# Performance work log

Measured on AMD Instinct MI355X. Metric: run time of the kernel, lower is better.

Reference implementation:

```python
import jax, jax.numpy as jnp
import numpy as np

B, C_IN, N = 8, 512, 4096   # batch, input channels, timesteps
D, K = 256, 2048            # code dim (n_out), codebook size (vq_n_embed)
EMA_G = 0.99                # vq_ema_gamma


def setup_inputs() -> dict:
    key = jax.random.key(0)
    k1, k2, k3 = jax.random.split(key, 3)
    z = jax.random.normal(k1, (B, C_IN, N), jnp.float32)
    # emb: xavier_uniform with gain=10 over (K, D)
    eb = 10.0 * np.sqrt(6.0 / (K + D))
    emb = jax.random.uniform(k2, (K, D), jnp.float32, -eb, eb)
    # 1x1 Conv1d weight (no bias), xavier_uniform over (D, C_IN)
    wb = np.sqrt(6.0 / (D + C_IN))
    W = jax.random.uniform(k3, (D, C_IN), jnp.float32, -wb, wb)
    # EMA buffers as initialized in __init__
    ema_numer = emb * (1.0 - EMA_G)
    ema_denom = jnp.ones((K,), jnp.float32) * (1.0 - EMA_G)
    return {"z": z, "W": W, "emb": emb, "ema_numer": ema_numer, "ema_denom": ema_denom}


def reference(z, W, emb, ema_numer, ema_denom):
    # 1x1 conv (no bias): ze (B, D, N)
    ze = jnp.einsum('dc,bcn->bdn', W, z)
    e = jax.lax.stop_gradient(emb)  # sg(emb)
    # Squared L2 distances (B, K, N) via ||ze||^2 + ||e||^2 - 2 e.ze
    # (mathematically equal to the broadcasted (ze-e)^2 sum, without the
    #  huge (B,K,D,N) intermediate)
    ze_sq = jnp.sum(ze * ze, axis=1)              # (B, N)
    e_sq = jnp.sum(e * e, axis=1)                 # (K,)
    cross = jnp.einsum('kd,bdn->bkn', e, ze)      # (B, K, N)
    d2 = ze_sq[:, None, :] + e_sq[None, :, None] - 2.0 * cross
    min_ind = jnp.argmin(d2, axis=1)              # (B, N) int
    zq = jnp.take(e, min_ind, axis=0).transpose(0, 2, 1)  # (B, D, N)
    # ReplaceGrad straight-through: value = zq, gradient flows to ze
    out = ze + jax.lax.stop_gradient(zq - ze)
    # EMA codebook statistics (scatter-add over assignments)
    flat_ind = min_ind.reshape(-1)                          # (B*N,)
    flat_ze = ze.transpose(0, 2, 1).reshape(-1, D)          # (B*N, D)
    z_sum = jax.ops.segment_sum(flat_ze, flat_ind, num_segments=K)
    n_sum = jax.ops.segment_sum(jnp.ones((flat_ind.shape[0],), ze.dtype), flat_ind, num_segments=K)
    ema_numer_new = EMA_G * ema_numer + (1.0 - EMA_G) * z_sum
    ema_denom_new = EMA_G * ema_denom + (1.0 - EMA_G) * n_sum
    return out, ema_numer_new, ema_denom_new
```

## Files before the change

kernel.cpp:

```cpp
#include <hip/hip_runtime.h>

#define B_   8
#define CIN  512
#define NN_  4096
#define DD   256
#define KK   2048
#define KSPLIT 4
#define KPER (KK / KSPLIT)
#define NG   (B_ * NN_)

typedef _Float16 f16x8 __attribute__((ext_vector_type(8)));
typedef _Float16 f16x4 __attribute__((ext_vector_type(4)));
typedef float    f32x16 __attribute__((ext_vector_type(16)));

#define MFMA16 __builtin_amdgcn_mfma_f32_32x32x16_f16

#define GLDS16(gp, lp) __builtin_amdgcn_global_load_lds( \
    (const __attribute__((address_space(1))) void*)(gp), \
    (__attribute__((address_space(3))) void*)(lp), 16, 0, 0)

__global__ __launch_bounds__(256) void k_esq(const float* __restrict__ emb,
                                             float* __restrict__ esq,
                                             _Float16* __restrict__ emb_h,
                                             _Float16* __restrict__ emb_l) {
  int t = threadIdx.x;
  int lane = t & 63;
  int k = blockIdx.x * 4 + (t >> 6);
  float4 v = *(const float4*)&emb[(size_t)k * DD + 4 * lane];
  float s = v.x * v.x + v.y * v.y + v.z * v.z + v.w * v.w;
  f16x4 h, l;
  float* vp = (float*)&v;
#pragma unroll
  for (int i = 0; i < 4; i++) {
    _Float16 hh = (_Float16)vp[i];
    h[i] = hh;
    l[i] = (_Float16)(vp[i] - (float)hh);
  }
  *(f16x4*)&emb_h[(size_t)k * DD + 4 * lane] = h;
  *(f16x4*)&emb_l[(size_t)k * DD + 4 * lane] = l;
  for (int off = 32; off > 0; off >>= 1) s += __shfl_down(s, off, 64);
  if (lane == 0) esq[k] = s;
}

__global__ __launch_bounds__(256) void k_ze(const float* __restrict__ W,
                                            const float* __restrict__ z,
                                            _Float16* __restrict__ zeT_h,
                                            _Float16* __restrict__ zeT_l) {
  __shared__ __align__(16) char sm[67584];
  const int t = threadIdx.x;
  const int w = t >> 6, lane = t & 63;
  const int lr = lane & 31, lh = lane >> 5;
  const int wm = w & 1, wn = w >> 1;
  const int swz = (lr >> 1) & 3;
  const int b = blockIdx.z, d0 = blockIdx.y * 128, n0 = blockIdx.x * 128;
  const float* zb = z + (size_t)b * CIN * NN_ + n0;

  _Float16* Ah = (_Float16*)sm;
  _Float16* Al = (_Float16*)(sm + 16384);
  float*    Zs = (float*)(sm + 32768);

  auto stageA = [&](int buf, int c0) {
#pragma unroll
    for (int i = 0; i < 4; i++) {
      int fid = i * 256 + t;
      int d = fid >> 3, q8 = fid & 7;
      float4 v = *(const float4*)&W[(size_t)(d0 + d) * CIN + c0 + 4 * q8];
      float* vp = (float*)&v;
      f16x4 h, l;
#pragma unroll
      for (int e = 0; e < 4; e++) {
        _Float16 hh = (_Float16)vp[e];
        h[e] = hh;
        l[e] = (_Float16)(vp[e] - (float)hh);
      }
      int p16 = (q8 >> 1) ^ ((d >> 1) & 3);
      int off = (buf * 128 + d) * 32 + p16 * 8 + (q8 & 1) * 4;
      *(f16x4*)&Ah[off] = h;
      *(f16x4*)&Al[off] = l;
    }
  };
  auto stageZ = [&](int buf, int c0) {
#pragma unroll
    for (int i = 0; i < 4; i++) {
      int r = 8 * w + 2 * i;
      float* lbase = Zs + (size_t)buf * 4096 + r * 128;
      const float* gp = zb + (size_t)(c0 + r + lh) * NN_ + 4 * lr;
      GLDS16(gp, lbase);
    }
  };

  f32x16 acc[2][2];
#pragma unroll
  for (int mt = 0; mt < 2; mt++)
#pragma unroll
    for (int nt = 0; nt < 2; nt++)
#pragma unroll
      for (int i = 0; i < 16; i++) acc[mt][nt][i] = 0.0f;

  stageA(0, 0);
  stageZ(0, 0);
  int buf = 0;
  for (int c0 = 0; c0 < CIN; c0 += 32) {
    __syncthreads();
    if (c0 + 32 < CIN) { stageA(buf ^ 1, c0 + 32); stageZ(buf ^ 1, c0 + 32); }
    const _Float16* AhB = Ah + (size_t)buf * 128 * 32;
    const _Float16* AlB = Al + (size_t)buf * 128 * 32;
    const float*    ZsB = Zs + (size_t)buf * 4096;
#pragma unroll
    for (int s = 0; s < 2; s++) {
      const int cbase = 16 * s + 8 * lh;
      const int pa = (2 * s + lh) ^ swz;
      const int aoff = pa * 8;
      f16x8 ah0 = *(const f16x8*)&AhB[(wm * 64 + lr) * 32 + aoff];
      f16x8 ah1 = *(const f16x8*)&AhB[(wm * 64 + 32 + lr) * 32 + aoff];
      f16x8 al0 = *(const f16x8*)&AlB[(wm * 64 + lr) * 32 + aoff];
      f16x8 al1 = *(const f16x8*)&AlB[(wm * 64 + 32 + lr) * 32 + aoff];
      f16x8 bh0, bl0, bh1, bl1;
#pragma unroll
      for (int j = 0; j < 8; j++) {
        float x0 = ZsB[(cbase + j) * 128 + wn * 64 + lr];
        float x1 = ZsB[(cbase + j) * 128 + wn * 64 + 32 + lr];
        _Float16 h0 = (_Float16)x0;
        bh0[j] = h0;
        bl0[j] = (_Float16)(x0 - (float)h0);
        _Float16 h1 = (_Float16)x1;
        bh1[j] = h1;
        bl1[j] = (_Float16)(x1 - (float)h1);
      }
      acc[0][0] = MFMA16(ah0, bh0, acc[0][0], 0, 0, 0);
      acc[0][1] = MFMA16(ah0, bh1, acc[0][1], 0, 0, 0);
      acc[1][0] = MFMA16(ah1, bh0, acc[1][0], 0, 0, 0);
      acc[1][1] = MFMA16(ah1, bh1, acc[1][1], 0, 0, 0);
      acc[0][0] = MFMA16(ah0, bl0, acc[0][0], 0, 0, 0);
      acc[0][1] = MFMA16(ah0, bl1, acc[0][1], 0, 0, 0);
      acc[1][0] = MFMA16(ah1, bl0, acc[1][0], 0, 0, 0);
      acc[1][1] = MFMA16(ah1, bl1, acc[1][1], 0, 0, 0);
      acc[0][0] = MFMA16(al0, bh0, acc[0][0], 0, 0, 0);
      acc[0][1] = MFMA16(al0, bh1, acc[0][1], 0, 0, 0);
      acc[1][0] = MFMA16(al1, bh0, acc[1][0], 0, 0, 0);
      acc[1][1] = MFMA16(al1, bh1, acc[1][1], 0, 0, 0);
    }
    buf ^= 1;
  }

  __syncthreads();
  _Float16* Eh = (_Float16*)sm;
  _Float16* El = (_Float16*)(sm + 33792);
#pragma unroll
  for (int mt = 0; mt < 2; mt++)
#pragma unroll
    for (int nt = 0; nt < 2; nt++) {
      int n_l = wn * 64 + nt * 32 + lr;
#pragma unroll
      for (int g = 0; g < 4; g++) {
        int d_l = wm * 64 + mt * 32 + 8 * g + 4 * lh;
        f16x4 h, l;
#pragma unroll
        for (int e = 0; e < 4; e++) {
          float x = acc[mt][nt][4 * g + e];
          _Float16 hh = (_Float16)x;
          h[e] = hh;
          l[e] = (_Float16)(x - (float)hh);
        }
        *(f16x4*)&Eh[n_l * 132 + d_l] = h;
        *(f16x4*)&El[n_l * 132 + d_l] = l;
      }
    }
  __syncthreads();
  _Float16* gh = zeT_h + ((size_t)b * NN_ + n0) * DD + d0;
  _Float16* gl = zeT_l + ((size_t)b * NN_ + n0) * DD + d0;
#pragma unroll
  for (int i = 0; i < 16; i++) {
    int n = i * 8 + w * 2 + lh;
    int d = 4 * lr;
    *(f16x4*)&gh[(size_t)n * DD + d] = *(const f16x4*)&Eh[n * 132 + d];
    *(f16x4*)&gl[(size_t)n * DD + d] = *(const f16x4*)&El[n * 132 + d];
  }
}

__global__ __launch_bounds__(256) void k_argmin(const _Float16* __restrict__ emb_h,
                                                const _Float16* __restrict__ emb_l,
                                                const _Float16* __restrict__ zeT_h,
                                                const _Float16* __restrict__ zeT_l,
                                                const float* __restrict__ esq,
                                                float* __restrict__ pval,
                                                int* __restrict__ pidx) {
  __shared__ __align__(16) char sm[69632];
  const int t = threadIdx.x;
  const int w = t >> 6, lane = t & 63;
  const int lr = lane & 31, lh = lane >> 5;
  const int wm = w & 1, wn = w >> 1;
  const int swz = (lr >> 1) & 3;
  const int b = blockIdx.y, n0 = blockIdx.x * 128, ks = blockIdx.z;
  const int kbase = ks * KPER;

  float* esqs = (float*)(sm + 65536);
  *(float2*)&esqs[2 * t] = *(const float2*)&esq[kbase + 2 * t];

  const _Float16* zb_h = zeT_h + ((size_t)b * NN_ + n0) * DD;
  const _Float16* zb_l = zeT_l + ((size_t)b * NN_ + n0) * DD;

  auto stage = [&](int buf, int kt, int dc) {
    const int k0 = kbase + kt * 128;
    const int q = lane & 3, rr = lane >> 2;
    const int g = q ^ ((rr >> 1) & 3);
    const int rb0 = 32 * w;
#pragma unroll
    for (int j = 0; j < 2; j++) {
      int rb = rb0 + 16 * j;
      int r = rb + rr;
      int col = dc + 8 * g;
      size_t eo = (size_t)(k0 + r) * DD + col;
      size_t zo = (size_t)r * DD + col;
      char* lb = sm + (size_t)buf * 8192 + rb * 64;
      GLDS16(emb_h + eo, lb);
      GLDS16(emb_l + eo, lb + 16384);
      GLDS16(zb_h + zo, lb + 32768);
      GLDS16(zb_l + zo, lb + 49152);
    }
  };

  f32x16 vzero;
#pragma unroll
  for (int i = 0; i < 16; i++) vzero[i] = 0.0f;

  float bestv[2];
  int   besti[2];
  bestv[0] = bestv[1] = 3.4e38f;
  besti[0] = besti[1] = 0;

  stage(0, 0, 0);
  int buf = 0;
  for (int kt = 0; kt < 4; kt++) {
    f32x16 acc00 = vzero, acc01 = vzero, acc10 = vzero, acc11 = vzero;
    for (int dc = 0; dc < DD; dc += 32) {
      __syncthreads();
      if (dc + 32 < DD) stage(buf ^ 1, kt, dc + 32);
      else if (kt < 3) stage(buf ^ 1, kt + 1, 0);
      const _Float16* EHb = (const _Float16*)(sm + buf * 8192);
      const _Float16* ELb = (const _Float16*)(sm + 16384 + buf * 8192);
      const _Float16* ZHb = (const _Float16*)(sm + 32768 + buf * 8192);
      const _Float16* ZLb = (const _Float16*)(sm + 49152 + buf * 8192);
#pragma unroll
      for (int s = 0; s < 2; s++) {
        const int p = (2 * s + lh) ^ swz;
        const int acol = p * 8;
        const int ar0 = (wm * 64 + lr) * 32 + acol;
        const int ar1 = (wm * 64 + 32 + lr) * 32 + acol;
        const int br0 = (wn * 64 + lr) * 32 + acol;
        const int br1 = (wn * 64 + 32 + lr) * 32 + acol;
        f16x8 ah0 = *(const f16x8*)(EHb + ar0);
        f16x8 ah1 = *(const f16x8*)(EHb + ar1);
        f16x8 al0 = *(const f16x8*)(ELb + ar0);
        f16x8 al1 = *(const f16x8*)(ELb + ar1);
        f16x8 bh0 = *(const f16x8*)(ZHb + br0);
        f16x8 bh1 = *(const f16x8*)(ZHb + br1);
        f16x8 bl0 = *(const f16x8*)(ZLb + br0);
        f16x8 bl1 = *(const f16x8*)(ZLb + br1);
        acc00 = MFMA16(ah0, bh0, acc00, 0, 0, 0);
        acc01 = MFMA16(ah0, bh1, acc01, 0, 0, 0);
        acc10 = MFMA16(ah1, bh0, acc10, 0, 0, 0);
        acc11 = MFMA16(ah1, bh1, acc11, 0, 0, 0);
        acc00 = MFMA16(ah0, bl0, acc00, 0, 0, 0);
        acc01 = MFMA16(ah0, bl1, acc01, 0, 0, 0);
        acc10 = MFMA16(ah1, bl0, acc10, 0, 0, 0);
        acc11 = MFMA16(ah1, bl1, acc11, 0, 0, 0);
        acc00 = MFMA16(al0, bh0, acc00, 0, 0, 0);
        acc01 = MFMA16(al0, bh1, acc01, 0, 0, 0);
        acc10 = MFMA16(al1, bh0, acc10, 0, 0, 0);
        acc11 = MFMA16(al1, bh1, acc11, 0, 0, 0);
      }
      buf ^= 1;
    }
#pragma unroll
    for (int mt = 0; mt < 2; mt++)
#pragma unroll
      for (int nt = 0; nt < 2; nt++) {
        const f32x16& a = (mt == 0) ? (nt == 0 ? acc00 : acc01)
                                    : (nt == 0 ? acc10 : acc11);
#pragma unroll
        for (int r = 0; r < 16; r++) {
          int kl = kt * 128 + wm * 64 + mt * 32 + (r & 3) + 8 * (r >> 2) + 4 * lh;
          float d2 = esqs[kl] - 2.0f * a[r];
          int kg = kbase + kl;
          if (d2 < bestv[nt] || (d2 == bestv[nt] && kg < besti[nt])) {
            bestv[nt] = d2; besti[nt] = kg;
          }
        }
      }
  }

#pragma unroll
  for (int nt = 0; nt < 2; nt++) {
    float ov = __shfl_xor(bestv[nt], 32, 64);
    int   oi = __shfl_xor(besti[nt], 32, 64);
    if (ov < bestv[nt] || (ov == bestv[nt] && oi < besti[nt])) {
      bestv[nt] = ov; besti[nt] = oi;
    }
  }
  float* pv = (float*)(sm + 67584);
  int*   pi = (int*)(sm + 68608);
  __syncthreads();
  if (lh == 0) {
#pragma unroll
    for (int nt = 0; nt < 2; nt++) {
      pv[(w * 2 + nt) * 32 + lr] = bestv[nt];
      pi[(w * 2 + nt) * 32 + lr] = besti[nt];
    }
  }
  __syncthreads();
  if (t < 128) {
    int wn2 = t >> 6, nt = (t >> 5) & 1, nl = t & 31;
    int i0 = ((2 * wn2 + 0) * 2 + nt) * 32 + nl;
    int i1 = ((2 * wn2 + 1) * 2 + nt) * 32 + nl;
    float v0 = pv[i0], v1 = pv[i1];
    int   j0 = pi[i0], j1 = pi[i1];
    if (v1 < v0 || (v1 == v0 && j1 < j0)) { v0 = v1; j0 = j1; }
    size_t o = ((size_t)ks * B_ + b) * NN_ + n0 + t;
    pval[o] = v0;
    pidx[o] = j0;
  }
}

__global__ __launch_bounds__(256) void k_histm(const float* __restrict__ pval,
                                               const int* __restrict__ pidx,
                                               int* __restrict__ mind,
                                               int* __restrict__ hist) {
  __shared__ int h[KK];
  const int t = threadIdx.x;
#pragma unroll
  for (int i = 0; i < 8; i++) h[t + 256 * i] = 0;
  __syncthreads();
  const int base = blockIdx.x * 2048;
#pragma unroll
  for (int i = 0; i < 8; i++) {
    int g = base + i * 256 + t;
    float bv = pval[g];
    int   bi = pidx[g];
#pragma unroll
    for (int ks = 1; ks < KSPLIT; ks++) {
      float v = pval[(size_t)ks * NG + g];
      int  ii = pidx[(size_t)ks * NG + g];
      if (v < bv || (v == bv && ii < bi)) { bv = v; bi = ii; }
    }
    mind[g] = bi;
    atomicAdd(&h[bi], 1);
  }
  __syncthreads();
#pragma unroll
  for (int i = 0; i < 8; i++) {
    int v = h[t + 256 * i];
    if (v) atomicAdd(&hist[t + 256 * i], v);
  }
}

__global__ __launch_bounds__(256) void k_scan(const int* __restrict__ hist,
                                              int* __restrict__ cursor,
                                              float* __restrict__ nsumf) {
  __shared__ int ps[256];
  const int t = threadIdx.x;
  int c[8], s = 0;
#pragma unroll
  for (int e = 0; e < 8; e++) { c[e] = hist[8 * t + e]; s += c[e]; }
  ps[t] = s;
  __syncthreads();
  for (int off = 1; off < 256; off <<= 1) {
    int v = (t >= off) ? ps[t - off] : 0;
    __syncthreads();
    ps[t] += v;
    __syncthreads();
  }
  int run = ps[t] - s;
#pragma unroll
  for (int e = 0; e < 8; e++) {
    cursor[8 * t + e] = run;
    nsumf[8 * t + e] = (float)c[e];
    run += c[e];
  }
}

__global__ __launch_bounds__(256) void k_pos(const int* __restrict__ mind,
                                             int* __restrict__ cursor,
                                             int* __restrict__ sortp) {
  int g = blockIdx.x * 256 + threadIdx.x;
  int k = mind[g];
  int p = atomicAdd(&cursor[k], 1);
  sortp[p] = (k << 15) | g;
}

__global__ __launch_bounds__(256) void k_out(const float* __restrict__ emb,
                                             const int* __restrict__ mind,
                                             float* __restrict__ out) {
  __shared__ __align__(16) float E[64][257];
  __shared__ int idxl[64];
  const int t = threadIdx.x;
  const int b  = blockIdx.y;
  const int n0 = blockIdx.x * 64;
  if (t < 64) idxl[t] = mind[(size_t)b * NN_ + n0 + t];
  __syncthreads();

  for (int i = 0; i < 16; i++) {
    int cid = t + 256 * i;
    int r = cid >> 6, q = cid & 63;
    float4 v = *(const float4*)&emb[(size_t)idxl[r] * DD + 4 * q];
    float* vp = (float*)&v;
    E[r][4 * q + 0] = vp[0];
    E[r][4 * q + 1] = vp[1];
    E[r][4 * q + 2] = vp[2];
    E[r][4 * q + 3] = vp[3];
  }
  __syncthreads();
  const int nq = t & 15, dg = t >> 4;
  float* outb = out + (size_t)b * DD * NN_ + n0;
#pragma unroll
  for (int i = 0; i < 16; i++) {
    int d = i * 16 + dg;
    float4 v = make_float4(E[4 * nq + 0][d], E[4 * nq + 1][d],
                           E[4 * nq + 2][d], E[4 * nq + 3][d]);
    *(float4*)&outb[(size_t)d * NN_ + 4 * nq] = v;
  }
}

__global__ __launch_bounds__(256) void k_zsum(const int* __restrict__ sortp,
                                              const _Float16* __restrict__ zeT_h,
                                              const _Float16* __restrict__ zeT_l,
                                              float* __restrict__ z_sum) {
  __shared__ int sg[256];
  const int t = threadIdx.x;
  const int w = t >> 6, lane = t & 63;
  sg[t] = sortp[blockIdx.x * 256 + t];
  __syncthreads();
  const int base = w * 64;
  float acc[4] = {0.f, 0.f, 0.f, 0.f};
  int cur = sg[base] >> 15;
  for (int j = 0; j < 64; j++) {
    int e = sg[base + j];
    int k = e >> 15, g = e & 32767;
    if (k != cur) {
      float* zs = &z_sum[(size_t)cur * DD + 4 * lane];
#pragma unroll
      for (int x = 0; x < 4; x++) { atomicAdd(&zs[x], acc[x]); acc[x] = 0.f; }
      cur = k;
    }
    f16x4 h = *(const f16x4*)&zeT_h[(size_t)g * DD + 4 * lane];
    f16x4 l = *(const f16x4*)&zeT_l[(size_t)g * DD + 4 * lane];
#pragma unroll
    for (int x = 0; x < 4; x++) acc[x] += (float)h[x] + (float)l[x];
  }
  float* zs = &z_sum[(size_t)cur * DD + 4 * lane];
#pragma unroll
  for (int x = 0; x < 4; x++) atomicAdd(&zs[x], acc[x]);
}

__global__ __launch_bounds__(256) void k_ema(const float* __restrict__ ema_numer,
                                             const float* __restrict__ ema_denom,
                                             const float* __restrict__ z_sum,
                                             const float* __restrict__ nsumf,
                                             float* __restrict__ out_numer,
                                             float* __restrict__ out_denom) {
  const float G  = 0.99f;
  const float OG = 0.009999999776482582f;
  int i = blockIdx.x * 256 + threadIdx.x;
  if (i < KK * DD) {
    out_numer[i] = G * ema_numer[i] + OG * z_sum[i];
  } else {
    int j = i - KK * DD;
    if (j < KK) out_denom[j] = G * ema_denom[j] + OG * nsumf[j];
  }
}

extern "C" void kernel_launch(void* const* d_in, const int* in_sizes, int n_in,
                              void* d_out, int out_size, void* d_ws, size_t ws_size,
                              hipStream_t stream) {
  (void)in_sizes; (void)n_in; (void)out_size; (void)ws_size;
  const float* z         = (const float*)d_in[0];
  const float* W         = (const float*)d_in[1];
  const float* emb       = (const float*)d_in[2];
  const float* ema_numer = (const float*)d_in[3];
  const float* ema_denom = (const float*)d_in[4];

  float* out       = (float*)d_out;
  float* out_numer = out + (size_t)B_ * DD * NN_;
  float* out_denom = out_numer + (size_t)KK * DD;

  const size_t ZET = (size_t)B_ * NN_ * DD;
  _Float16* zeT_h = (_Float16*)d_ws;
  _Float16* zeT_l = zeT_h + ZET;
  float* esq    = (float*)(zeT_l + ZET);
  float* zsum   = esq + KK;
  int*   hist   = (int*)(zsum + (size_t)KK * DD);
  int*   cursor = hist + KK;
  float* nsumf  = (float*)(cursor + KK);
  float* pval   = nsumf + KK;
  int*   pidx   = (int*)(pval + (size_t)KSPLIT * NG);
  int*   mind   = pidx + (size_t)KSPLIT * NG;
  int*   sortp  = mind + NG;
  _Float16* emb_h = (_Float16*)(sortp + NG);
  _Float16* emb_l = emb_h + (size_t)KK * DD;

  hipMemsetAsync(zsum, 0, (size_t)(KK * DD + KK) * sizeof(float), stream);

  k_esq<<<dim3(KK / 4), 256, 0, stream>>>(emb, esq, emb_h, emb_l);
  k_ze<<<dim3(NN_ / 128, DD / 128, B_), 256, 0, stream>>>(W, z, zeT_h, zeT_l);
  k_argmin<<<dim3(NN_ / 128, B_, KSPLIT), 256, 0, stream>>>(emb_h, emb_l, zeT_h, zeT_l,
                                                            esq, pval, pidx);
  k_histm<<<dim3(NG / 2048), 256, 0, stream>>>(pval, pidx, mind, hist);
  k_scan<<<dim3(1), 256, 0, stream>>>(hist, cursor, nsumf);
  k_pos<<<dim3(NG / 256), 256, 0, stream>>>(mind, cursor, sortp);
  k_out<<<dim3(NN_ / 64, B_), 256, 0, stream>>>(emb, mind, out);
  k_zsum<<<dim3(NG / 256), 256, 0, stream>>>(sortp, zeT_h, zeT_l, zsum);
  k_ema<<<dim3((KK * DD + KK) / 256), 256, 0, stream>>>(ema_numer, ema_denom, zsum, nsumf,
                                                        out_numer, out_denom);
}
```

Measured before the change: 307.4 us.

## Load ze operand directly from global into registers, halve LDS footprint

The argmin GEMM kernel stops staging the ze (B operand) tiles through LDS and instead has each lane load its MFMA fragments straight from global memory into double-buffered registers, prefetched one step ahead. Only the codebook tiles remain in LDS, which cuts shared memory per block from about 68KB to 36KB and could allow more resident blocks per CU. The trade-off is more register pressure and uncoalesced or duplicated global reads, since both wm waves fetch the same B fragments, though caches may absorb that.

```diff
diff --git a/kernel.cpp b/kernel.cpp
--- a/kernel.cpp
+++ b/kernel.cpp
@@ -185,7 +185,7 @@
                                                 const float* __restrict__ esq,
                                                 float* __restrict__ pval,
                                                 int* __restrict__ pidx) {
-  __shared__ __align__(16) char sm[69632];
+  __shared__ __align__(16) char sm[36864];
   const int t = threadIdx.x;
   const int w = t >> 6, lane = t & 63;
   const int lr = lane & 31, lh = lane >> 5;
@@ -194,13 +194,17 @@
   const int b = blockIdx.y, n0 = blockIdx.x * 128, ks = blockIdx.z;
   const int kbase = ks * KPER;
 
-  float* esqs = (float*)(sm + 65536);
+  float* esqs = (float*)(sm + 32768);
   *(float2*)&esqs[2 * t] = *(const float2*)&esq[kbase + 2 * t];
 
   const _Float16* zb_h = zeT_h + ((size_t)b * NN_ + n0) * DD;
   const _Float16* zb_l = zeT_l + ((size_t)b * NN_ + n0) * DD;
-
-  auto stage = [&](int buf, int kt, int dc) {
+  const _Float16* pB0h = zb_h + (size_t)(wn * 64 + lr) * DD + 8 * lh;
+  const _Float16* pB1h = pB0h + 32 * DD;
+  const _Float16* pB0l = zb_l + (size_t)(wn * 64 + lr) * DD + 8 * lh;
+  const _Float16* pB1l = pB0l + 32 * DD;
+
+  auto stageE = [&](int buf, int kt, int dc) {
     const int k0 = kbase + kt * 128;
     const int q = lane & 3, rr = lane >> 2;
     const int g = q ^ ((rr >> 1) & 3);
@@ -209,14 +213,19 @@
     for (int j = 0; j < 2; j++) {
       int rb = rb0 + 16 * j;
       int r = rb + rr;
-      int col = dc + 8 * g;
-      size_t eo = (size_t)(k0 + r) * DD + col;
-      size_t zo = (size_t)r * DD + col;
+      size_t eo = (size_t)(k0 + r) * DD + dc + 8 * g;
       char* lb = sm + (size_t)buf * 8192 + rb * 64;
       GLDS16(emb_h + eo, lb);
       GLDS16(emb_l + eo, lb + 16384);
-      GLDS16(zb_h + zo, lb + 32768);
-      GLDS16(zb_l + zo, lb + 49152);
+    }
+  };
+  auto loadB = [&](f16x8* bh, f16x8* bl, int dc) {
+#pragma unroll
+    for (int s = 0; s < 2; s++) {
+      bh[2 * s + 0] = *(const f16x8*)(pB0h + dc + 16 * s);
+      bh[2 * s + 1] = *(const f16x8*)(pB1h + dc + 16 * s);
+      bl[2 * s + 0] = *(const f16x8*)(pB0l + dc + 16 * s);
+      bl[2 * s + 1] = *(const f16x8*)(pB1l + dc + 16 * s);
     }
   };
 
@@ -229,34 +238,39 @@
   bestv[0] = bestv[1] = 3.4e38f;
   besti[0] = besti[1] = 0;
 
-  stage(0, 0, 0);
-  int buf = 0;
+  f16x8 B0h[4], B0l[4], B1h[4], B1l[4];
+
+  stageE(0, 0, 0);
+  loadB(B0h, B0l, 0);
   for (int kt = 0; kt < 4; kt++) {
     f32x16 acc00 = vzero, acc01 = vzero, acc10 = vzero, acc11 = vzero;
-    for (int dc = 0; dc < DD; dc += 32) {
+#pragma unroll
+    for (int i = 0; i < 8; i++) {
+      const int dc = i * 32;
+      const int cbuf = i & 1;
       __syncthreads();
-      if (dc + 32 < DD) stage(buf ^ 1, kt, dc + 32);
-      else if (kt < 3) stage(buf ^ 1, kt + 1, 0);
-      const _Float16* EHb = (const _Float16*)(sm + buf * 8192);
-      const _Float16* ELb = (const _Float16*)(sm + 16384 + buf * 8192);
-      const _Float16* ZHb = (const _Float16*)(sm + 32768 + buf * 8192);
-      const _Float16* ZLb = (const _Float16*)(sm + 49152 + buf * 8192);
+      if (dc + 32 < DD) {
+        stageE(cbuf ^ 1, kt, dc + 32);
+        loadB(cbuf ? B0h : B1h, cbuf ? B0l : B1l, dc + 32);
+      } else if (kt < 3) {
+        stageE(cbuf ^ 1, kt + 1, 0);
+        loadB(cbuf ? B0h : B1h, cbuf ? B0l : B1l, 0);
+      }
+      const _Float16* EHb = (const _Float16*)(sm + cbuf * 8192);
+      const _Float16* ELb = (const _Float16*)(sm + 16384 + cbuf * 8192);
+      const f16x8* bhc = cbuf ? B1h : B0h;
+      const f16x8* blc = cbuf ? B1l : B0l;
 #pragma unroll
       for (int s = 0; s < 2; s++) {
-        const int p = (2 * s + lh) ^ swz;
-        const int acol = p * 8;
-        const int ar0 = (wm * 64 + lr) * 32 + acol;
-        const int ar1 = (wm * 64 + 32 + lr) * 32 + acol;
-        const int br0 = (wn * 64 + lr) * 32 + acol;
-        const int br1 = (wn * 64 + 32 + lr) * 32 + acol;
+        const int pa = (2 * s + lh) ^ swz;
+        const int ar0 = (wm * 64 + lr) * 32 + pa * 8;
+        const int ar1 = (wm * 64 + 32 + lr) * 32 + pa * 8;
         f16x8 ah0 = *(const f16x8*)(EHb + ar0);
         f16x8 ah1 = *(const f16x8*)(EHb + ar1);
         f16x8 al0 = *(const f16x8*)(ELb + ar0);
         f16x8 al1 = *(const f16x8*)(ELb + ar1);
-        f16x8 bh0 = *(const f16x8*)(ZHb + br0);
-        f16x8 bh1 = *(const f16x8*)(ZHb + br1);
-        f16x8 bl0 = *(const f16x8*)(ZLb + br0);
-        f16x8 bl1 = *(const f16x8*)(ZLb + br1);
+        f16x8 bh0 = bhc[2 * s + 0], bh1 = bhc[2 * s + 1];
+        f16x8 bl0 = blc[2 * s + 0], bl1 = blc[2 * s + 1];
         acc00 = MFMA16(ah0, bh0, acc00, 0, 0, 0);
         acc01 = MFMA16(ah0, bh1, acc01, 0, 0, 0);
         acc10 = MFMA16(ah1, bh0, acc10, 0, 0, 0);
@@ -270,7 +284,6 @@
         acc10 = MFMA16(al1, bh0, acc10, 0, 0, 0);
         acc11 = MFMA16(al1, bh1, acc11, 0, 0, 0);
       }
-      buf ^= 1;
     }
 #pragma unroll
     for (int mt = 0; mt < 2; mt++)
@@ -298,8 +311,8 @@
       bestv[nt] = ov; besti[nt] = oi;
     }
   }
-  float* pv = (float*)(sm + 67584);
-  int*   pi = (int*)(sm + 68608);
+  float* pv = (float*)(sm + 34816);
+  int*   pi = (int*)(sm + 35840);
   __syncthreads();
   if (lh == 0) {
 #pragma unroll
```

New measurement: 337.4 us. 9.8% more time.
